# Kernel optimization log

Hardware: AMD Instinct MI355X
Metric: run time of the kernel (lower is better)

The kernel has to match this reference:

```python
import jax, jax.numpy as jnp
import numpy as np

E = 768      # embed_dim (hidden_size)
H = 12       # num_attention_heads
DH = E // H  # head_dim = 64
B, S = 8, 1024


def setup_inputs() -> dict:
    key = jax.random.key(0)
    ks = jax.random.split(key, 10)
    sc = 1.0 / np.sqrt(E)
    inp = {
        "hidden_state": jax.random.normal(ks[0], (B, S, E), dtype=jnp.float32),
        # per-head Q/K/V projections, stacked over heads: [H, E, DH]
        "Wq": jax.random.normal(ks[1], (H, E, DH), dtype=jnp.float32) * sc,
        "bq": jax.random.normal(ks[2], (H, DH), dtype=jnp.float32) * 0.02,
        "Wk": jax.random.normal(ks[3], (H, E, DH), dtype=jnp.float32) * sc,
        "bk": jax.random.normal(ks[4], (H, DH), dtype=jnp.float32) * 0.02,
        "Wv": jax.random.normal(ks[5], (H, E, DH), dtype=jnp.float32) * sc,
        "bv": jax.random.normal(ks[6], (H, DH), dtype=jnp.float32) * 0.02,
        # output projection: [E, E]
        "Wo": jax.random.normal(ks[7], (E, E), dtype=jnp.float32) * sc,
        "bo": jax.random.normal(ks[8], (E,), dtype=jnp.float32) * 0.02,
    }
    return inp


def reference(hidden_state, Wq, bq, Wk, bk, Wv, bv, Wo, bo):
    # Q/K/V per head: [B,S,E] x [H,E,D] -> [B,H,S,D]
    q = jnp.einsum("bse,hed->bhsd", hidden_state, Wq) + bq[None, :, None, :]
    k = jnp.einsum("bse,hed->bhsd", hidden_state, Wk) + bk[None, :, None, :]
    v = jnp.einsum("bse,hed->bhsd", hidden_state, Wv) + bv[None, :, None, :]
    scale = 1.0 / jnp.sqrt(jnp.asarray(DH, dtype=q.dtype))
    scores = jnp.einsum("bhsd,bhtd->bhst", q, k) * scale   # [B,H,S,S]
    weights = jax.nn.softmax(scores, axis=-1)
    attn = jnp.einsum("bhst,bhtd->bhsd", weights, v)        # [B,H,S,D]
    # concat heads (head order matches ModuleList concat): [B,S,H*D]=[B,S,E]
    x = attn.transpose(0, 2, 1, 3).reshape(hidden_state.shape[0], hidden_state.shape[1], E)
    return x @ Wo + bo
```

## Files before the change

kernel.cpp:

```cpp
#include <hip/hip_runtime.h>

typedef unsigned short u16;
typedef __bf16 bf16;
typedef bf16 bf16x8 __attribute__((ext_vector_type(8)));
typedef float f32x4 __attribute__((ext_vector_type(4)));
typedef u16 u16x4 __attribute__((ext_vector_type(4)));
typedef u16 u16x8 __attribute__((ext_vector_type(8)));

#define MROWS 8192
#define EDIM 768
#define NQKV 2304
#define NHEAD 12
#define DH 64
#define SEQ 1024
#define BATCH 8
#define BH 96
#define BHSD (BH * SEQ * DH)
#define KIT64 (EDIM / 64)

#if __has_builtin(__builtin_amdgcn_exp2f)
#define EXP2(x) __builtin_amdgcn_exp2f(x)
#else
#define EXP2(x) exp2f(x)
#endif

__device__ __forceinline__ u16 f2bf(float f) {
  bf16 b = (bf16)f;
  return __builtin_bit_cast(u16, b);
}

__device__ __forceinline__ void gload_lds16(const u16* g, u16* l) {
  __builtin_amdgcn_global_load_lds(
      (const __attribute__((address_space(1))) void*)g,
      (__attribute__((address_space(3))) void*)l, 16, 0, 0);
}


__global__ void cvt_x(const float* __restrict__ x, u16* __restrict__ xb, int n) {
  int i = (blockIdx.x * blockDim.x + threadIdx.x) * 4;
  if (i >= n) return;
  float4 v = *(const float4*)(x + i);
  u16x4 o;
  o[0] = f2bf(v.x); o[1] = f2bf(v.y); o[2] = f2bf(v.z); o[3] = f2bf(v.w);
  *(u16x4*)(xb + i) = o;
}

__global__ __launch_bounds__(256) void pack_w(
    const float* __restrict__ Wq, const float* __restrict__ Wk,
    const float* __restrict__ Wv, const float* __restrict__ Wo,
    u16* __restrict__ Wt, u16* __restrict__ Wot) {
  __shared__ float T[64][65];
  int bid = blockIdx.x;
  int tid = threadIdx.x;
  int c = tid & 63, r4 = tid >> 6;
  if (bid < 432) {
    int region = bid / 144, rem = bid - region * 144;
    int h = rem / 12, e0 = (rem - h * 12) * 64;
    const float* W = region == 0 ? Wq : (region == 1 ? Wk : Wv);
    for (int p = 0; p < 16; p++) {
      int er = r4 + p * 4;
      T[er][c] = W[(size_t)(h * EDIM + e0 + er) * DH + c];
    }
    __syncthreads();
    int nbase = region * EDIM + h * 64;
    for (int p = 0; p < 16; p++) {
      int dr = r4 + p * 4;
      Wt[(size_t)(nbase + dr) * EDIM + e0 + c] = f2bf(T[c][dr]);
    }
  } else {
    bid -= 432;
    int n0 = (bid / 12) * 64, e0 = (bid - (bid / 12) * 12) * 64;
    for (int p = 0; p < 16; p++) {
      int er = r4 + p * 4;
      T[er][c] = Wo[(size_t)(e0 + er) * EDIM + n0 + c];
    }
    __syncthreads();
    for (int p = 0; p < 16; p++) {
      int dr = r4 + p * 4;
      Wot[(size_t)(n0 + dr) * EDIM + e0 + c] = f2bf(T[c][dr]);
    }
  }
}

__device__ __forceinline__ void gemm_core64(
    const u16* __restrict__ A, const u16* __restrict__ Bt,
    u16* As, u16* Bs,
    int m0, int n0, int tid, f32x4 acc[4][4]) {
  int wv = __builtin_amdgcn_readfirstlane(tid >> 6);
  int lane = tid & 63, quad = lane >> 4, l16 = lane & 15;
  int wm = (wv & 1) * 64, wn = (wv >> 1) * 64;
  int lr = lane >> 3, cpos = lane & 7;
  int swcol = (cpos ^ lr) * 8;
  const u16* Ag = A + (size_t)(m0 + wv * 32 + lr) * EDIM + swcol;
  const u16* Bg = Bt + (size_t)(n0 + wv * 32 + lr) * EDIM + swcol;
  u16* Asl = As + (wv * 32 + lr) * 64 + cpos * 8;
  u16* Bsl = Bs + (wv * 32 + lr) * 64 + cpos * 8;

  for (int k = 0; k < KIT64; k++) {
    __syncthreads();
    const u16* ak = Ag + k * 64;
    const u16* bk = Bg + k * 64;
#pragma unroll
    for (int q = 0; q < 4; q++) {
      gload_lds16(ak + q * 8 * EDIM, Asl + q * 512);
      gload_lds16(bk + q * 8 * EDIM, Bsl + q * 512);
    }
    __syncthreads();
#pragma unroll
    for (int kh = 0; kh < 2; kh++) {
      bf16x8 af[4], bfr[4];
      for (int i = 0; i < 4; i++) {
        int row = wm + i * 16 + l16;
        af[i] = *(const bf16x8*)(As + row * 64 + (((kh * 4 + quad) ^ (row & 7))) * 8);
      }
      for (int j = 0; j < 4; j++) {
        int row = wn + j * 16 + l16;
        bfr[j] = *(const bf16x8*)(Bs + row * 64 + (((kh * 4 + quad) ^ (row & 7))) * 8);
      }
      for (int i = 0; i < 4; i++)
        for (int j = 0; j < 4; j++)
          acc[i][j] = __builtin_amdgcn_mfma_f32_16x16x32_bf16(af[i], bfr[j], acc[i][j], 0, 0, 0);
    }
  }
}

__global__ __launch_bounds__(256, 4) void gemm_qkv(
    const u16* __restrict__ A, const u16* __restrict__ Bt,
    const float* __restrict__ bq, const float* __restrict__ bk, const float* __restrict__ bv,
    u16* __restrict__ qkv) {
  __shared__ __align__(16) u16 As[128 * 64];
  __shared__ __align__(16) u16 Bs[128 * 64];
  int tid = threadIdx.x;
  int wv = tid >> 6, lane = tid & 63, quad = lane >> 4, l16 = lane & 15;
  int wm = (wv & 1) * 64, wn = (wv >> 1) * 64;
  int m0 = blockIdx.x * 128, n0 = blockIdx.y * 128;
  f32x4 acc[4][4] = {};
  gemm_core64(A, Bt, As, Bs, m0, n0, tid, acc);

  const float kQscale = 0.18033688011112042f;
  for (int i = 0; i < 4; i++) {
    int row0 = m0 + wm + i * 16 + quad * 4;
    for (int j = 0; j < 4; j++) {
      int n = n0 + wn + j * 16 + l16;
      int region = n / EDIM;
      int hd = n - region * EDIM;
      int h = hd >> 6, d = hd & 63;
      const float* bp = region == 0 ? bq : (region == 1 ? bk : bv);
      float bias = bp[hd];
      float scale = region == 0 ? kQscale : 1.0f;
      for (int r = 0; r < 4; r++) {
        int rr = row0 + r;
        int bb = rr >> 10, s = rr & 1023;
        float val = (acc[i][j][r] + bias) * scale;
        u16 bv16 = f2bf(val);
        int bhh = bb * NHEAD + h;
        if (region < 2) {
          qkv[(size_t)region * BHSD + ((size_t)bhh * SEQ + s) * DH + d] = bv16;
        } else {
          qkv[(size_t)2 * BHSD + ((size_t)bhh * DH + d) * SEQ + s] = bv16;
        }
      }
    }
  }
}

__global__ __launch_bounds__(256, 4) void attn_kernel(const u16* __restrict__ qkv, u16* __restrict__ attn) {
  int bh = blockIdx.x;
  int b = bh / NHEAD, h = bh - b * NHEAD;
  const u16* Q  = qkv + (size_t)bh * SEQ * DH;
  const u16* K  = qkv + (size_t)(BH + bh) * SEQ * DH;
  const u16* VT = qkv + (size_t)(2 * BH + bh) * SEQ * DH;
  int tid = threadIdx.x, wave = tid >> 6, lane = tid & 63, quad = lane >> 4, l16 = lane & 15;
  int q_base = blockIdx.y * 64 + wave * 16;

  __shared__ u16 Ks[64 * 72];
  __shared__ u16 Vts[80 * 72];
  __shared__ u16 Ps[4][16 * 72];

  for (int i = tid; i < 16 * 64; i += 256) {
    int rr = i >> 6, cc = i & 63;
    Vts[(64 + rr) * 72 + cc] = (rr == 0) ? (u16)0x3F80 : (u16)0;
  }

  bf16x8 qf[2];
  for (int c = 0; c < 2; c++)
    qf[c] = *(const bf16x8*)(Q + (size_t)(q_base + l16) * DH + c * 32 + quad * 8);

  f32x4 o[4] = {};
  f32x4 o5 = {};

  int tr = tid >> 3, tc8 = (tid & 7) * 8;

  u16x8 kv0 = *(const u16x8*)(K + (size_t)tr * DH + tc8);
  u16x8 kv1 = *(const u16x8*)(K + (size_t)(32 + tr) * DH + tc8);
  u16x8 vv0 = *(const u16x8*)(VT + (size_t)tr * SEQ + tc8);
  u16x8 vv1 = *(const u16x8*)(VT + (size_t)(32 + tr) * SEQ + tc8);

  for (int t0 = 0; t0 < SEQ; t0 += 64) {
    __syncthreads();
    *(u16x8*)(Ks + tr * 72 + tc8) = kv0;
    *(u16x8*)(Ks + (tr + 32) * 72 + tc8) = kv1;
    *(u16x8*)(Vts + tr * 72 + tc8) = vv0;
    *(u16x8*)(Vts + (tr + 32) * 72 + tc8) = vv1;
    __syncthreads();
    if (t0 + 64 < SEQ) {
      kv0 = *(const u16x8*)(K + (size_t)(t0 + 64 + tr) * DH + tc8);
      kv1 = *(const u16x8*)(K + (size_t)(t0 + 96 + tr) * DH + tc8);
      vv0 = *(const u16x8*)(VT + (size_t)tr * SEQ + t0 + 64 + tc8);
      vv1 = *(const u16x8*)(VT + (size_t)(32 + tr) * SEQ + t0 + 64 + tc8);
    }

    float p[4][4];
    for (int tc = 0; tc < 4; tc++) {
      bf16x8 kf0 = *(const bf16x8*)(Ks + (tc * 16 + l16) * 72 + quad * 8);
      bf16x8 kf1 = *(const bf16x8*)(Ks + (tc * 16 + l16) * 72 + 32 + quad * 8);
      f32x4 z = {};
      z = __builtin_amdgcn_mfma_f32_16x16x32_bf16(qf[0], kf0, z, 0, 0, 0);
      z = __builtin_amdgcn_mfma_f32_16x16x32_bf16(qf[1], kf1, z, 0, 0, 0);
      for (int r = 0; r < 4; r++)
        p[tc][r] = EXP2(z[r]);
    }

    u16* P = Ps[wave];
    for (int tc = 0; tc < 4; tc++)
      for (int r = 0; r < 4; r++)
        P[(quad * 4 + r) * 72 + tc * 16 + l16] = f2bf(p[tc][r]);
    bf16x8 pf[2];
    for (int kc = 0; kc < 2; kc++)
      pf[kc] = *(const bf16x8*)(P + l16 * 72 + kc * 32 + quad * 8);

    for (int n = 0; n < 4; n++) {
      bf16x8 vf0 = *(const bf16x8*)(Vts + (n * 16 + l16) * 72 + quad * 8);
      bf16x8 vf1 = *(const bf16x8*)(Vts + (n * 16 + l16) * 72 + 32 + quad * 8);
      o[n] = __builtin_amdgcn_mfma_f32_16x16x32_bf16(pf[0], vf0, o[n], 0, 0, 0);
      o[n] = __builtin_amdgcn_mfma_f32_16x16x32_bf16(pf[1], vf1, o[n], 0, 0, 0);
    }
    bf16x8 v50 = *(const bf16x8*)(Vts + (64 + l16) * 72 + quad * 8);
    bf16x8 v51 = *(const bf16x8*)(Vts + (64 + l16) * 72 + 32 + quad * 8);
    o5 = __builtin_amdgcn_mfma_f32_16x16x32_bf16(pf[0], v50, o5, 0, 0, 0);
    o5 = __builtin_amdgcn_mfma_f32_16x16x32_bf16(pf[1], v51, o5, 0, 0, 0);
  }

  for (int r = 0; r < 4; r++) {
    float s = __shfl(o5[r], quad << 4);
    float inv = 1.0f / s;
    int qrow = q_base + quad * 4 + r;
    size_t rowoff = (size_t)(b * SEQ + qrow) * EDIM + h * DH;
    for (int n = 0; n < 4; n++)
      attn[rowoff + n * 16 + l16] = f2bf(o[n][r] * inv);
  }
}

__global__ __launch_bounds__(256, 4) void gemm_out(
    const u16* __restrict__ A, const u16* __restrict__ Bt,
    const float* __restrict__ bo, float* __restrict__ out) {
  __shared__ __align__(16) u16 As[128 * 64];
  __shared__ __align__(16) u16 Bs[128 * 64];
  int tid = threadIdx.x;
  int wv = tid >> 6, lane = tid & 63, quad = lane >> 4, l16 = lane & 15;
  int wm = (wv & 1) * 64, wn = (wv >> 1) * 64;
  int m0 = blockIdx.x * 128, n0 = blockIdx.y * 128;
  f32x4 acc[4][4] = {};
  gemm_core64(A, Bt, As, Bs, m0, n0, tid, acc);

  for (int i = 0; i < 4; i++) {
    int row0 = m0 + wm + i * 16 + quad * 4;
    for (int j = 0; j < 4; j++) {
      int n = n0 + wn + j * 16 + l16;
      float bias = bo[n];
      for (int r = 0; r < 4; r++)
        out[(size_t)(row0 + r) * EDIM + n] = acc[i][j][r] + bias;
    }
  }
}

extern "C" void kernel_launch(void* const* d_in, const int* in_sizes, int n_in,
                              void* d_out, int out_size, void* d_ws, size_t ws_size,
                              hipStream_t stream) {
  const float* x  = (const float*)d_in[0];
  const float* Wq = (const float*)d_in[1];
  const float* bq = (const float*)d_in[2];
  const float* Wk = (const float*)d_in[3];
  const float* bk = (const float*)d_in[4];
  const float* Wv = (const float*)d_in[5];
  const float* bv = (const float*)d_in[6];
  const float* Wo = (const float*)d_in[7];
  const float* bo = (const float*)d_in[8];
  float* out = (float*)d_out;
  char* ws = (char*)d_ws;

  u16* Xb   = (u16*)(ws);
  u16* Wt   = (u16*)(ws + 12582912);
  u16* Wot  = (u16*)(ws + 16121856);
  u16* qkv  = (u16*)(ws + 17301504);
  u16* attn = (u16*)(ws + 55050240);

  cvt_x<<<6144, 256, 0, stream>>>(x, Xb, MROWS * EDIM);
  pack_w<<<576, 256, 0, stream>>>(Wq, Wk, Wv, Wo, Wt, Wot);
  gemm_qkv<<<dim3(64, 18), 256, 0, stream>>>(Xb, Wt, bq, bk, bv, qkv);
  attn_kernel<<<dim3(96, 16), 256, 0, stream>>>(qkv, attn);
  gemm_out<<<dim3(64, 6), 256, 0, stream>>>(attn, Wot, bo, out);
}
```

Baseline: 218.1 us.

## Remap blocks per XCD, swizzle attention LDS, compute softmax sums in registers

```diff
diff --git a/kernel.cpp b/kernel.cpp
--- a/kernel.cpp
+++ b/kernel.cpp
@@ -133,7 +133,10 @@
   int tid = threadIdx.x;
   int wv = tid >> 6, lane = tid & 63, quad = lane >> 4, l16 = lane & 15;
   int wm = (wv & 1) * 64, wn = (wv >> 1) * 64;
-  int m0 = blockIdx.x * 128, n0 = blockIdx.y * 128;
+  int lin = blockIdx.y * 64 + blockIdx.x;
+  int xcd = lin & 7, r8 = lin >> 3;
+  int m0 = (xcd * 8 + (r8 & 7)) * 128;
+  int n0 = (r8 >> 3) * 128;
   f32x4 acc[4][4] = {};
   gemm_core64(A, Bt, As, Bs, m0, n0, tid, acc);
 
@@ -164,32 +167,36 @@
   }
 }
 
-__global__ __launch_bounds__(256, 4) void attn_kernel(const u16* __restrict__ qkv, u16* __restrict__ attn) {
-  int bh = blockIdx.x;
+__global__ __launch_bounds__(256, 6) void attn_kernel(const u16* __restrict__ qkv, u16* __restrict__ attn) {
+  int lin = blockIdx.y * 96 + blockIdx.x;
+  int xcd = lin & 7, rr6 = lin >> 3;
+  int bh = xcd * 12 + (rr6 >> 4);
+  int qt = rr6 & 15;
   int b = bh / NHEAD, h = bh - b * NHEAD;
   const u16* Q  = qkv + (size_t)bh * SEQ * DH;
   const u16* K  = qkv + (size_t)(BH + bh) * SEQ * DH;
   const u16* VT = qkv + (size_t)(2 * BH + bh) * SEQ * DH;
   int tid = threadIdx.x, wave = tid >> 6, lane = tid & 63, quad = lane >> 4, l16 = lane & 15;
-  int q_base = blockIdx.y * 64 + wave * 16;
-
-  __shared__ u16 Ks[64 * 72];
-  __shared__ u16 Vts[80 * 72];
-  __shared__ u16 Ps[4][16 * 72];
-
-  for (int i = tid; i < 16 * 64; i += 256) {
-    int rr = i >> 6, cc = i & 63;
-    Vts[(64 + rr) * 72 + cc] = (rr == 0) ? (u16)0x3F80 : (u16)0;
-  }
+  int q_base = qt * 64 + wave * 16;
+
+  __shared__ u16 Ks[64 * 64];
+  __shared__ u16 Vts[64 * 64];
+  __shared__ u16 Ps[4][16 * 64];
 
   bf16x8 qf[2];
   for (int c = 0; c < 2; c++)
     qf[c] = *(const bf16x8*)(Q + (size_t)(q_base + l16) * DH + c * 32 + quad * 8);
 
   f32x4 o[4] = {};
-  f32x4 o5 = {};
-
-  int tr = tid >> 3, tc8 = (tid & 7) * 8;
+  float psum[4] = {};
+
+  int tr = tid >> 3, cpos = tid & 7;
+  int ssw = (cpos ^ (tr & 7)) * 8;
+  u16* KsW0 = Ks + tr * 64 + ssw;
+  u16* KsW1 = Ks + (tr + 32) * 64 + ssw;
+  u16* VsW0 = Vts + tr * 64 + ssw;
+  u16* VsW1 = Vts + (tr + 32) * 64 + ssw;
+  int tc8 = cpos * 8;
 
   u16x8 kv0 = *(const u16x8*)(K + (size_t)tr * DH + tc8);
   u16x8 kv1 = *(const u16x8*)(K + (size_t)(32 + tr) * DH + tc8);
@@ -198,10 +205,10 @@
 
   for (int t0 = 0; t0 < SEQ; t0 += 64) {
     __syncthreads();
-    *(u16x8*)(Ks + tr * 72 + tc8) = kv0;
-    *(u16x8*)(Ks + (tr + 32) * 72 + tc8) = kv1;
-    *(u16x8*)(Vts + tr * 72 + tc8) = vv0;
-    *(u16x8*)(Vts + (tr + 32) * 72 + tc8) = vv1;
+    *(u16x8*)KsW0 = kv0;
+    *(u16x8*)KsW1 = kv1;
+    *(u16x8*)VsW0 = vv0;
+    *(u16x8*)VsW1 = vv1;
     __syncthreads();
     if (t0 + 64 < SEQ) {
       kv0 = *(const u16x8*)(K + (size_t)(t0 + 64 + tr) * DH + tc8);
@@ -212,38 +219,44 @@
 
     float p[4][4];
     for (int tc = 0; tc < 4; tc++) {
-      bf16x8 kf0 = *(const bf16x8*)(Ks + (tc * 16 + l16) * 72 + quad * 8);
-      bf16x8 kf1 = *(const bf16x8*)(Ks + (tc * 16 + l16) * 72 + 32 + quad * 8);
+      int krow = tc * 16 + l16, k7 = l16 & 7;
+      bf16x8 kf0 = *(const bf16x8*)(Ks + krow * 64 + ((quad ^ k7) * 8));
+      bf16x8 kf1 = *(const bf16x8*)(Ks + krow * 64 + (((4 + quad) ^ k7) * 8));
       f32x4 z = {};
       z = __builtin_amdgcn_mfma_f32_16x16x32_bf16(qf[0], kf0, z, 0, 0, 0);
       z = __builtin_amdgcn_mfma_f32_16x16x32_bf16(qf[1], kf1, z, 0, 0, 0);
-      for (int r = 0; r < 4; r++)
+      for (int r = 0; r < 4; r++) {
         p[tc][r] = EXP2(z[r]);
+        psum[r] += p[tc][r];
+      }
     }
 
     u16* P = Ps[wave];
     for (int tc = 0; tc < 4; tc++)
-      for (int r = 0; r < 4; r++)
-        P[(quad * 4 + r) * 72 + tc * 16 + l16] = f2bf(p[tc][r]);
+      for (int r = 0; r < 4; r++) {
+        int prow = quad * 4 + r;
+        int pc = tc * 2 + (l16 >> 3);
+        P[prow * 64 + ((pc ^ (prow & 7)) * 8) + (l16 & 7)] = f2bf(p[tc][r]);
+      }
     bf16x8 pf[2];
     for (int kc = 0; kc < 2; kc++)
-      pf[kc] = *(const bf16x8*)(P + l16 * 72 + kc * 32 + quad * 8);
+      pf[kc] = *(const bf16x8*)(Ps[wave] + l16 * 64 + (((kc * 4 + quad) ^ (l16 & 7)) * 8));
 
     for (int n = 0; n < 4; n++) {
-      bf16x8 vf0 = *(const bf16x8*)(Vts + (n * 16 + l16) * 72 + quad * 8);
-      bf16x8 vf1 = *(const bf16x8*)(Vts + (n * 16 + l16) * 72 + 32 + quad * 8);
+      int vrow = n * 16 + l16, v7 = l16 & 7;
+      bf16x8 vf0 = *(const bf16x8*)(Vts + vrow * 64 + ((quad ^ v7) * 8));
+      bf16x8 vf1 = *(const bf16x8*)(Vts + vrow * 64 + (((4 + quad) ^ v7) * 8));
       o[n] = __builtin_amdgcn_mfma_f32_16x16x32_bf16(pf[0], vf0, o[n], 0, 0, 0);
       o[n] = __builtin_amdgcn_mfma_f32_16x16x32_bf16(pf[1], vf1, o[n], 0, 0, 0);
     }
-    bf16x8 v50 = *(const bf16x8*)(Vts + (64 + l16) * 72 + quad * 8);
-    bf16x8 v51 = *(const bf16x8*)(Vts + (64 + l16) * 72 + 32 + quad * 8);
-    o5 = __builtin_amdgcn_mfma_f32_16x16x32_bf16(pf[0], v50, o5, 0, 0, 0);
-    o5 = __builtin_amdgcn_mfma_f32_16x16x32_bf16(pf[1], v51, o5, 0, 0, 0);
-  }
+  }
+
+  for (int m = 1; m < 16; m <<= 1)
+    for (int r = 0; r < 4; r++)
+      psum[r] += __shfl_xor(psum[r], m);
 
   for (int r = 0; r < 4; r++) {
-    float s = __shfl(o5[r], quad << 4);
-    float inv = 1.0f / s;
+    float inv = 1.0f / psum[r];
     int qrow = q_base + quad * 4 + r;
     size_t rowoff = (size_t)(b * SEQ + qrow) * EDIM + h * DH;
     for (int n = 0; n < 4; n++)
@@ -259,7 +272,10 @@
   int tid = threadIdx.x;
   int wv = tid >> 6, lane = tid & 63, quad = lane >> 4, l16 = lane & 15;
   int wm = (wv & 1) * 64, wn = (wv >> 1) * 64;
-  int m0 = blockIdx.x * 128, n0 = blockIdx.y * 128;
+  int lin = blockIdx.y * 64 + blockIdx.x;
+  int xcd = lin & 7, r8 = lin >> 3;
+  int m0 = (xcd * 8 + (r8 & 7)) * 128;
+  int n0 = (r8 >> 3) * 128;
   f32x4 acc[4][4] = {};
   gemm_core64(A, Bt, As, Bs, m0, n0, tid, acc);
 
```

New measurement: 229.1 us. 5.0% more time.
